# Performance work log

Measured on AMD Instinct MI355X. Metric: run time of the kernel, lower is better.

## Reference

```python
import jax, jax.numpy as jnp
import numpy as np

IN_DIM = 128
OUT_DIM = 128
NUM_INTERVALS = 8
SPLINE_ORDER = 3
BATCH = 1024


def make_grids():
    # domain [-1, 1] for every (in, out) pair, extended by spline_order knots each side
    step = 2.0 / NUM_INTERVALS
    G = NUM_INTERVALS + 2 * SPLINE_ORDER + 1
    g = (-1.0 - SPLINE_ORDER * step) + jnp.arange(G, dtype=jnp.float32) * step  # [G]
    return jnp.broadcast_to(g, (IN_DIM, OUT_DIM, G))


def setup_inputs() -> dict:
    key = jax.random.key(0)
    k1, k2, k3 = jax.random.split(key, 3)
    x = jax.random.normal(k1, (BATCH, IN_DIM), dtype=jnp.float32)
    n_cp = NUM_INTERVALS + SPLINE_ORDER
    control_points = 0.1 * jax.random.normal(k2, (IN_DIM, OUT_DIM, n_cp), dtype=jnp.float32)
    scaling_factors = np.sqrt(2.0 / OUT_DIM).astype(np.float32) * jax.random.normal(
        k3, (IN_DIM, OUT_DIM), dtype=jnp.float32)
    grids = make_grids()
    return {"x": x, "control_points": control_points,
            "scaling_factors": scaling_factors, "grids": grids}


def bspline_bases(x, grids, k):
    # Bottom-up Cox-de-Boor DP (identical recurrence to the naive top-down version).
    # x: [B, in], grids: [in, out, G] -> returns all degree-k bases [B, in, out, G-1-k]
    ex = x[:, :, None, None]          # [B, in, 1, 1]
    t = grids[None]                   # [1, in, out, G]
    B = ((t[..., :-1] <= ex) & (ex < t[..., 1:])).astype(x.dtype)  # degree 0
    for d in range(1, k + 1):
        tl  = t[..., : -(d + 1)]      # t[i]
        tr  = t[..., d:-1]            # t[i+d]
        tl1 = t[..., 1:-d]            # t[i+1]
        tr1 = t[..., d + 1:]          # t[i+d+1]
        B = (ex - tl) / (tr - tl) * B[..., :-1] + (tr1 - ex) / (tr1 - tl1) * B[..., 1:]
    return B


def reference(x, control_points, scaling_factors, grids):
    Bk = bspline_bases(x, grids, SPLINE_ORDER)                 # [B, in, out, n_cp]
    spline = jnp.einsum('biog,iog->bio', Bk, control_points)    # [B, in, out]
    res = scaling_factors[None] * (jax.nn.silu(x)[:, :, None] + spline)
    return jnp.sum(res, axis=1).astype(jnp.float32)             # [B, out]
```

## Files before the change

### kernel.cpp

```cpp
#include <hip/hip_runtime.h>
#include <math.h>


#define IN_DIM   128
#define OUT_DIM  128
#define NCP      11
#define GK       15
#define FS       12
#define KTOT     (IN_DIM * FS)
#define BT       8
#define OT       32
#define KS       8
#define THREADS  256

__global__ __launch_bounds__(256)
void kan_prep(const float* __restrict__ CP,
              const float* __restrict__ SF,
              float* __restrict__ W)
{
    const int p = blockIdx.x * 256 + threadIdx.x;
    const int i = p >> 7;
    const int o = p & (OUT_DIM - 1);
    const float s = SF[p];
    const float* cp = CP + p * NCP;
    const int kb = i * FS;
    #pragma unroll
    for (int g = 0; g < NCP; ++g)
        W[(kb + g) * OUT_DIM + o] = s * cp[g];
    W[(kb + NCP) * OUT_DIM + o] = s;
}

__global__ __launch_bounds__(THREADS, 3)
void kan_main(const float* __restrict__ X,
              const float* __restrict__ GR,
              const float* __restrict__ W,
              float* __restrict__ OUT)
{
    __shared__ float F[BT * KTOT];

    const int tid = threadIdx.x;
    const int b0  = blockIdx.x * BT;
    const int o0  = blockIdx.y * OT;

    const float t0 = GR[0];
    const float h  = GR[1] - t0;
    const float r1 = 1.0f / h;
    const float r2 = 1.0f / (2.0f * h);
    const float r3 = 1.0f / (3.0f * h);
    float kn[GK];
    #pragma unroll
    for (int j = 0; j < GK; ++j) kn[j] = t0 + (float)j * h;

    #pragma unroll
    for (int kq = 0; kq < (BT * IN_DIM) / THREADS; ++kq) {
        const int p = tid + kq * THREADS;
        const int r = p >> 7;
        const int i = p & (IN_DIM - 1);

        const float x = X[(b0 + r) * IN_DIM + i];

        float b[GK - 1];
        #pragma unroll
        for (int j = 0; j < GK - 1; ++j)
            b[j] = (kn[j] <= x && x < kn[j + 1]) ? 1.0f : 0.0f;
        #pragma unroll
        for (int j = 0; j < GK - 2; ++j)
            b[j] = ((x - kn[j]) * b[j] + (kn[j + 2] - x) * b[j + 1]) * r1;
        #pragma unroll
        for (int j = 0; j < GK - 3; ++j)
            b[j] = ((x - kn[j]) * b[j] + (kn[j + 3] - x) * b[j + 1]) * r2;
        #pragma unroll
        for (int j = 0; j < GK - 4; ++j)
            b[j] = ((x - kn[j]) * b[j] + (kn[j + 4] - x) * b[j + 1]) * r3;

        const float silu = x / (1.0f + __expf(-x));

        float* f = &F[r * KTOT + i * FS];
        #pragma unroll
        for (int g = 0; g < NCP; ++g) f[g] = b[g];
        f[NCP] = silu;
    }
    __syncthreads();

    const int ol = tid & (OT - 1);
    const int ks = tid >> 5;
    const int o  = o0 + ol;

    float acc[BT];
    #pragma unroll
    for (int r = 0; r < BT; ++r) acc[r] = 0.0f;

    const int kbase = ks * (KTOT / KS);
    #pragma unroll 2
    for (int kk = 0; kk < KTOT / KS; kk += 4) {
        const int k = kbase + kk;
        const float w0 = W[(k + 0) * OUT_DIM + o];
        const float w1 = W[(k + 1) * OUT_DIM + o];
        const float w2 = W[(k + 2) * OUT_DIM + o];
        const float w3 = W[(k + 3) * OUT_DIM + o];
        #pragma unroll
        for (int r = 0; r < BT; ++r) {
            const float4 f = *(const float4*)&F[r * KTOT + k];
            acc[r] = fmaf(w0, f.x, acc[r]);
            acc[r] = fmaf(w1, f.y, acc[r]);
            acc[r] = fmaf(w2, f.z, acc[r]);
            acc[r] = fmaf(w3, f.w, acc[r]);
        }
    }

    __syncthreads();
    if (ks > 0) {
        #pragma unroll
        for (int r = 0; r < BT; ++r)
            F[((ks - 1) * BT + r) * OT + ol] = acc[r];
    }
    __syncthreads();
    if (ks == 0) {
        #pragma unroll
        for (int r = 0; r < BT; ++r) {
            float v = acc[r];
            #pragma unroll
            for (int q = 0; q < KS - 1; ++q)
                v += F[(q * BT + r) * OT + ol];
            OUT[(b0 + r) * OUT_DIM + o] = v;
        }
    }
}

extern "C" void kernel_launch(void* const* d_in, const int* in_sizes, int n_in,
                              void* d_out, int out_size, void* d_ws, size_t ws_size,
                              hipStream_t stream) {
    const float* x  = (const float*)d_in[0];
    const float* cp = (const float*)d_in[1];
    const float* sf = (const float*)d_in[2];
    const float* gr = (const float*)d_in[3];
    float* out = (float*)d_out;
    float* W   = (float*)d_ws;

    const int batch = in_sizes[0] / IN_DIM;

    kan_prep<<<(IN_DIM * OUT_DIM) / 256, 256, 0, stream>>>(cp, sf, W);
    dim3 grid(batch / BT, OUT_DIM / OT);
    kan_main<<<grid, THREADS, 0, stream>>>(x, gr, W, out);
}
```

Before: 76.61 us.

## Register-tile 4 outputs per thread with interleaved K split and vectorized LDS stores

Each thread now computes a 4-output by 8-row tile using float4 weight loads, and K is split 32 ways with an interleaved stride rather than 8 contiguous chunks. Basis values are written to shared memory as float4s. The final reduction is rewritten so all 256 threads sum 32 partials from a padded buffer. The aim is more FMAs per shared-memory load and wider global loads, at the cost of more registers (occupancy hint lowered to 2) and a larger cross-thread reduction.

```diff
diff --git a/kernel.cpp b/kernel.cpp
--- a/kernel.cpp
+++ b/kernel.cpp
@@ -10,8 +10,11 @@
 #define KTOT     (IN_DIM * FS)
 #define BT       8
 #define OT       32
-#define KS       8
+#define VO       4
+#define KSP      32
+#define NJ       12
 #define THREADS  256
+#define RPAD     260
 
 __global__ __launch_bounds__(256)
 void kan_prep(const float* __restrict__ CP,
@@ -30,7 +33,7 @@
     W[(kb + NCP) * OUT_DIM + o] = s;
 }
 
-__global__ __launch_bounds__(THREADS, 3)
+__global__ __launch_bounds__(THREADS, 2)
 void kan_main(const float* __restrict__ X,
               const float* __restrict__ GR,
               const float* __restrict__ W,
@@ -75,55 +78,70 @@
 
         const float silu = x / (1.0f + __expf(-x));
 
-        float* f = &F[r * KTOT + i * FS];
-        #pragma unroll
-        for (int g = 0; g < NCP; ++g) f[g] = b[g];
-        f[NCP] = silu;
+        float* f = &F[p * FS];
+        *(float4*)(f + 0) = make_float4(b[0], b[1], b[2], b[3]);
+        *(float4*)(f + 4) = make_float4(b[4], b[5], b[6], b[7]);
+        *(float4*)(f + 8) = make_float4(b[8], b[9], b[10], silu);
     }
     __syncthreads();
 
-    const int ol = tid & (OT - 1);
-    const int ks = tid >> 5;
-    const int o  = o0 + ol;
+    const int ol = tid & (OT / VO - 1);
+    const int ks = tid >> 3;
+    const int o4 = o0 + VO * ol;
 
-    float acc[BT];
+    float acc[BT][VO];
     #pragma unroll
-    for (int r = 0; r < BT; ++r) acc[r] = 0.0f;
+    for (int r = 0; r < BT; ++r)
+        #pragma unroll
+        for (int v = 0; v < VO; ++v) acc[r][v] = 0.0f;
 
-    const int kbase = ks * (KTOT / KS);
-    #pragma unroll 2
-    for (int kk = 0; kk < KTOT / KS; kk += 4) {
-        const int k = kbase + kk;
-        const float w0 = W[(k + 0) * OUT_DIM + o];
-        const float w1 = W[(k + 1) * OUT_DIM + o];
-        const float w2 = W[(k + 2) * OUT_DIM + o];
-        const float w3 = W[(k + 3) * OUT_DIM + o];
+    #pragma unroll
+    for (int j = 0; j < NJ; ++j) {
+        const int kg = 4 * (ks + KSP * j);
+
+        float4 w0 = *(const float4*)&W[(kg + 0) * OUT_DIM + o4];
+        float4 w1 = *(const float4*)&W[(kg + 1) * OUT_DIM + o4];
+        float4 w2 = *(const float4*)&W[(kg + 2) * OUT_DIM + o4];
+        float4 w3 = *(const float4*)&W[(kg + 3) * OUT_DIM + o4];
+
         #pragma unroll
         for (int r = 0; r < BT; ++r) {
-            const float4 f = *(const float4*)&F[r * KTOT + k];
-            acc[r] = fmaf(w0, f.x, acc[r]);
-            acc[r] = fmaf(w1, f.y, acc[r]);
-            acc[r] = fmaf(w2, f.z, acc[r]);
-            acc[r] = fmaf(w3, f.w, acc[r]);
+            const float4 f = *(const float4*)&F[r * KTOT + kg];
+            acc[r][0] = fmaf(f.x, w0.x, acc[r][0]);
+            acc[r][1] = fmaf(f.x, w0.y, acc[r][1]);
+            acc[r][2] = fmaf(f.x, w0.z, acc[r][2]);
+            acc[r][3] = fmaf(f.x, w0.w, acc[r][3]);
+            acc[r][0] = fmaf(f.y, w1.x, acc[r][0]);
+            acc[r][1] = fmaf(f.y, w1.y, acc[r][1]);
+            acc[r][2] = fmaf(f.y, w1.z, acc[r][2]);
+            acc[r][3] = fmaf(f.y, w1.w, acc[r][3]);
+            acc[r][0] = fmaf(f.z, w2.x, acc[r][0]);
+            acc[r][1] = fmaf(f.z, w2.y, acc[r][1]);
+            acc[r][2] = fmaf(f.z, w2.z, acc[r][2]);
+            acc[r][3] = fmaf(f.z, w2.w, acc[r][3]);
+            acc[r][0] = fmaf(f.w, w3.x, acc[r][0]);
+            acc[r][1] = fmaf(f.w, w3.y, acc[r][1]);
+            acc[r][2] = fmaf(f.w, w3.z, acc[r][2]);
+            acc[r][3] = fmaf(f.w, w3.w, acc[r][3]);
         }
     }
 
     __syncthreads();
-    if (ks > 0) {
+    float* red = F;
+    #pragma unroll
+    for (int r = 0; r < BT; ++r)
+        *(float4*)&red[ks * RPAD + r * OT + VO * ol] =
+            make_float4(acc[r][0], acc[r][1], acc[r][2], acc[r][3]);
+    __syncthreads();
+
+    {
+        const int r  = tid >> 5;
+        const int oc = tid & 31;
+        float v = 0.0f;
         #pragma unroll
-        for (int r = 0; r < BT; ++r)
-            F[((ks - 1) * BT + r) * OT + ol] = acc[r];
-    }
-    __syncthreads();
-    if (ks == 0) {
-        #pragma unroll
-        for (int r = 0; r < BT; ++r) {
-            float v = acc[r];
-            #pragma unroll
-            for (int q = 0; q < KS - 1; ++q)
-                v += F[(q * BT + r) * OT + ol];
-            OUT[(b0 + r) * OUT_DIM + o] = v;
-        }
+        for (int q = 0; q < KSP; ++q)
+            v += red[q * RPAD + r * OT + oc];
+        OUT[(b0 + r) * OUT_DIM + o0 + oc] = v;
     }
 }
 
```

Measured after the change: 69.07 us. -9.8%, faster.
